# Kernel optimization log

Measured on AMD Instinct MI355X. Metric: run time of the kernel, lower is better.

Reference implementation:

```python
import jax, jax.numpy as jnp
import numpy as np

FEAT = 256
HID = 256
HEADS = 4
DH = HID // HEADS
SCALE = DH ** (-0.5)


def _linear(x, W, b):
    # torch nn.Linear convention: W is [out, in]
    return jnp.einsum('...i,oi->...o', x, W) + b


def _layernorm(x, gamma, beta, eps=1e-5):
    mu = jnp.mean(x, axis=-1, keepdims=True)
    var = jnp.mean(jnp.square(x - mu), axis=-1, keepdims=True)
    return (x - mu) * jax.lax.rsqrt(var + eps) * gamma + beta


def setup_inputs() -> dict:
    key = jax.random.key(0)
    ks = jax.random.split(key, 16)
    B, N = 4, 2048
    def w(k, shape, fan_in):
        return jax.random.uniform(k, shape, jnp.float32, -1.0, 1.0) / np.sqrt(fan_in)
    return {
        'x0': jax.random.normal(ks[0], (B, N, FEAT), jnp.float32),
        'x1': jax.random.normal(ks[1], (B, N, FEAT), jnp.float32),
        'Wqk': w(ks[2], (HID, FEAT), FEAT), 'bqk': w(ks[3], (HID,), FEAT),
        'Wv': w(ks[4], (HID, FEAT), FEAT), 'bv': w(ks[5], (HID,), FEAT),
        'Wp': w(ks[6], (HID, HID), HID), 'bp': w(ks[7], (HID,), HID),
        'W1': w(ks[8], (FEAT * 2, FEAT + HID), FEAT + HID), 'b1': w(ks[9], (FEAT * 2,), FEAT + HID),
        'gamma': jnp.ones((FEAT * 2,), jnp.float32), 'beta': jnp.zeros((FEAT * 2,), jnp.float32),
        'W2': w(ks[10], (FEAT, FEAT * 2), FEAT * 2), 'b2': w(ks[11], (FEAT,), FEAT * 2),
    }


def _forward(x0, x1, Wqk, bqk, Wv, bv, Wp, bp, W1, b1, gamma, beta, W2, b2):
    B, N0, _ = x0.shape
    N1 = x1.shape[1]

    def heads(t):  # [B, N, HID] -> [B, H, N, DH]
        return t.reshape(t.shape[0], t.shape[1], HEADS, DH).transpose(0, 2, 1, 3)

    qk0 = heads(_linear(x0, Wqk, bqk)) * (SCALE ** 0.5)
    qk1 = heads(_linear(x1, Wqk, bqk)) * (SCALE ** 0.5)
    v0 = heads(_linear(x0, Wv, bv))
    v1 = heads(_linear(x1, Wv, bv))

    sim = jnp.einsum('bhid,bhjd->bhij', qk0, qk1)  # [B,H,N0,N1]
    attn01 = jax.nn.softmax(sim, axis=-1)                      # rows over N1
    attn10 = jax.nn.softmax(sim.transpose(0, 1, 3, 2), axis=-1)  # [B,H,N1,N0], rows over N0

    m0 = jnp.einsum('bhij,bhjd->bhid', attn01, v1)  # [B,H,N0,DH]
    m1 = jnp.einsum('bhij,bhjd->bhid', attn10, v0)  # [B,H,N1,DH]

    def merge(t):  # [B,H,N,DH] -> [B,N,HID]
        return t.transpose(0, 2, 1, 3).reshape(t.shape[0], t.shape[2], HID)

    m0 = _linear(merge(m0), Wp, bp)
    m1 = _linear(merge(m1), Wp, bp)

    def mlp(x, m):
        h = _linear(jnp.concatenate([x, m], axis=-1), W1, b1)
        h = jax.nn.gelu(_layernorm(h, gamma, beta), approximate=False)
        return x + _linear(h, W2, b2)

    return mlp(x0, m0), mlp(x1, m1)


def reference(x0, x1, Wqk, bqk, Wv, bv, Wp, bp, W1, b1, gamma, beta, W2, b2):
    return _forward(x0, x1, Wqk, bqk, Wv, bv, Wp, bp, W1, b1, gamma, beta, W2, b2)
```

## Files before the change

### kernel.cpp

```cpp
#include <hip/hip_runtime.h>
#include <hip/hip_bf16.h>
#include <math.h>

typedef __hip_bfloat16 hbf;
typedef __attribute__((ext_vector_type(8))) short short8;
typedef __attribute__((ext_vector_type(4))) short short4v;
typedef __attribute__((ext_vector_type(4))) float f32x4;

#define ROWS 8192
#define SQSL 0.4246609001440095f
#define COFF 24.0f

__device__ __forceinline__ short f2b(float f) {
    union { hbf h; short s; } u; u.h = __float2bfloat16(f); return u.s;
}
__device__ __forceinline__ float b2f(short s) {
    union { unsigned u; float f; } x;
    x.u = ((unsigned)(unsigned short)s) << 16; return x.f;
}

__global__ __launch_bounds__(256)
void prep(const float* __restrict__ Wqk, const float* __restrict__ Wv,
          const float* __restrict__ Wp, const float* __restrict__ W1,
          const float* __restrict__ W2,
          const float* __restrict__ bp, const float* __restrict__ b1,
          short* __restrict__ wq, short* __restrict__ wv,
          short* __restrict__ w1c, short* __restrict__ w2,
          float* __restrict__ bc)
{
    const int bid = blockIdx.x, tid = threadIdx.x;
    if (bid < 512) {
        const float* src; short* dst; int base; float sc = 1.f;
        if (bid < 64)       { src = Wqk; dst = wq; base = bid;       sc = SQSL; }
        else if (bid < 128) { src = Wv;  dst = wv; base = bid - 64; }
        else if (bid < 384) {
            int i = (bid - 128) * 256 + tid;
            int n = i >> 7, c = (i & 127) * 4;
            if (c < 256) {
                float4 f = ((const float4*)W1)[i];
                short4v s;
                s[0] = f2b(f.x); s[1] = f2b(f.y); s[2] = f2b(f.z); s[3] = f2b(f.w);
                *(short4v*)(w1c + (size_t)n * 512 + c) = s;
            }
            return;
        }
        else                { src = W2;  dst = w2; base = bid - 384; }
        int i = base * 256 + tid;
        float4 f = ((const float4*)src)[i];
        short4v s;
        s[0] = f2b(f.x * sc); s[1] = f2b(f.y * sc);
        s[2] = f2b(f.z * sc); s[3] = f2b(f.w * sc);
        *(short4v*)(dst + (size_t)i * 4) = s;
    } else if (bid < 1024) {
        int n = bid - 512;
        const float* wrow = W1 + (size_t)n * 512 + 256;
        float acc = 0.f;
        for (int k = 0; k < 256; ++k)
            acc += wrow[k] * Wp[(size_t)k * 256 + tid];
        w1c[(size_t)n * 512 + 256 + tid] = f2b(acc);
    } else {
        int n = (bid - 1024) * 256 + tid;
        const float* wrow = W1 + (size_t)n * 512 + 256;
        float acc = b1[n];
        for (int k = 0; k < 256; ++k) acc += wrow[k] * bp[k];
        bc[n] = acc;
    }
}

__global__ __launch_bounds__(256)
void gemm_qkv(const float* __restrict__ x0, const float* __restrict__ x1,
              const short* __restrict__ Wa, const short* __restrict__ Wb,
              const float* __restrict__ bias0, const float* __restrict__ bias1,
              short* __restrict__ qkb, short* __restrict__ vtb)
{
    const int fid  = blockIdx.x + (blockIdx.y << 2);
    const int col0 = (fid >> 8) * 128;
    const int row0 = (fid & 255) * 64;
    const int tid = threadIdx.x;
    const int lane = tid & 63, wave = tid >> 6;
    const int ln = lane & 15, quad = lane >> 4;
    const int wm = wave & 1, wn = wave >> 1;

    __shared__ short smem[64 * 72 + 128 * 72];
    short* As = smem;
    short* Bs = smem + 64 * 72;
    short* Vt = smem;

    const int ar = tid >> 2, ac = tid & 3;

    f32x4 acc[2][4];
    #pragma unroll
    for (int i = 0; i < 2; ++i)
        #pragma unroll
        for (int j = 0; j < 4; ++j) acc[i][j] = {0.f, 0.f, 0.f, 0.f};

    const short* wbase = (col0 < 256) ? Wa + (size_t)col0 * 256
                                      : Wb + (size_t)(col0 - 256) * 256;
    const float* xrow = (row0 + ar < ROWS)
        ? x0 + (size_t)(row0 + ar) * 256
        : x1 + (size_t)(row0 + ar - ROWS) * 256;

    float4 aF[4];
    short8 bR[4];
    #pragma unroll
    for (int i = 0; i < 4; ++i) aF[i] = ((const float4*)(xrow + ac * 16))[i];
    bR[0] = *(const short8*)(wbase + (size_t)ar * 256 + ac * 16);
    bR[1] = *(const short8*)(wbase + (size_t)ar * 256 + ac * 16 + 8);
    bR[2] = *(const short8*)(wbase + (size_t)(ar + 64) * 256 + ac * 16);
    bR[3] = *(const short8*)(wbase + (size_t)(ar + 64) * 256 + ac * 16 + 8);

    for (int k0 = 0; k0 < 256; k0 += 64) {
        {
            short8 s0, s1;
            s0[0] = f2b(aF[0].x); s0[1] = f2b(aF[0].y); s0[2] = f2b(aF[0].z); s0[3] = f2b(aF[0].w);
            s0[4] = f2b(aF[1].x); s0[5] = f2b(aF[1].y); s0[6] = f2b(aF[1].z); s0[7] = f2b(aF[1].w);
            s1[0] = f2b(aF[2].x); s1[1] = f2b(aF[2].y); s1[2] = f2b(aF[2].z); s1[3] = f2b(aF[2].w);
            s1[4] = f2b(aF[3].x); s1[5] = f2b(aF[3].y); s1[6] = f2b(aF[3].z); s1[7] = f2b(aF[3].w);
            *(short8*)&As[ar * 72 + ac * 16]     = s0;
            *(short8*)&As[ar * 72 + ac * 16 + 8] = s1;
        }
        *(short8*)&Bs[ar * 72 + ac * 16]            = bR[0];
        *(short8*)&Bs[ar * 72 + ac * 16 + 8]        = bR[1];
        *(short8*)&Bs[(ar + 64) * 72 + ac * 16]     = bR[2];
        *(short8*)&Bs[(ar + 64) * 72 + ac * 16 + 8] = bR[3];
        __syncthreads();

        if (k0 + 64 < 256) {
            const int kk = k0 + 64 + ac * 16;
            #pragma unroll
            for (int i = 0; i < 4; ++i) aF[i] = ((const float4*)(xrow + kk))[i];
            bR[0] = *(const short8*)(wbase + (size_t)ar * 256 + kk);
            bR[1] = *(const short8*)(wbase + (size_t)ar * 256 + kk + 8);
            bR[2] = *(const short8*)(wbase + (size_t)(ar + 64) * 256 + kk);
            bR[3] = *(const short8*)(wbase + (size_t)(ar + 64) * 256 + kk + 8);
        }

        short8 a[2][2], b[4][2];
        #pragma unroll
        for (int mi = 0; mi < 2; ++mi)
            #pragma unroll
            for (int ks = 0; ks < 2; ++ks)
                a[mi][ks] = *(const short8*)&As[(wm * 32 + mi * 16 + ln) * 72 + ks * 32 + quad * 8];
        #pragma unroll
        for (int nj = 0; nj < 4; ++nj)
            #pragma unroll
            for (int ks = 0; ks < 2; ++ks)
                b[nj][ks] = *(const short8*)&Bs[(wn * 64 + nj * 16 + ln) * 72 + ks * 32 + quad * 8];
        #pragma unroll
        for (int mi = 0; mi < 2; ++mi)
            #pragma unroll
            for (int nj = 0; nj < 4; ++nj) {
                acc[mi][nj] = __builtin_amdgcn_mfma_f32_16x16x32_bf16(
                                  b[nj][0], a[mi][0], acc[mi][nj], 0, 0, 0);
                acc[mi][nj] = __builtin_amdgcn_mfma_f32_16x16x32_bf16(
                                  b[nj][1], a[mi][1], acc[mi][nj], 0, 0, 0);
            }
        __syncthreads();
    }

    if (col0 < 256) {
        #pragma unroll
        for (int nj = 0; nj < 4; ++nj) {
            const int wcol = col0 + wn * 64 + nj * 16 + quad * 4;
            float4 bb = *(const float4*)(bias0 + wcol);
            #pragma unroll
            for (int mi = 0; mi < 2; ++mi) {
                const int tok = row0 + wm * 32 + mi * 16 + ln;
                f32x4 v = acc[mi][nj];
                short4v o;
                o[0] = f2b(fmaf(bb.x, SQSL, v[0]));
                o[1] = f2b(fmaf(bb.y, SQSL, v[1]));
                o[2] = f2b(fmaf(bb.z, SQSL, v[2]));
                o[3] = f2b(fmaf(bb.w, SQSL, v[3]));
                *(short4v*)(qkb + (size_t)tok * 256 + wcol) = o;
            }
        }
    } else {
        #pragma unroll
        for (int nj = 0; nj < 4; ++nj) {
            const int wrel = wn * 64 + nj * 16 + quad * 4;
            float4 bb = *(const float4*)(bias1 + (col0 - 256) + wrel);
            #pragma unroll
            for (int mi = 0; mi < 2; ++mi) {
                const int tl = wm * 32 + mi * 16 + ln;
                f32x4 v = acc[mi][nj];
                Vt[(wrel + 0) * 72 + tl] = f2b(v[0] + bb.x);
                Vt[(wrel + 1) * 72 + tl] = f2b(v[1] + bb.y);
                Vt[(wrel + 2) * 72 + tl] = f2b(v[2] + bb.z);
                Vt[(wrel + 3) * 72 + tl] = f2b(v[3] + bb.w);
            }
        }
        __syncthreads();
        {
            const int g4 = (row0 >> 11) * 4, tc0 = row0 & 2047;
            const int r = tid >> 1, hf = tid & 1;
            const int vcol = (col0 - 256) + r;
            const int hh = vcol >> 6, d = vcol & 63;
            short* dst = vtb + (size_t)((g4 + hh) * 64 + d) * 2048 + tc0 + hf * 32;
            #pragma unroll
            for (int cc = 0; cc < 4; ++cc)
                *(short8*)(dst + cc * 8) = *(const short8*)&Vt[r * 72 + hf * 32 + cc * 8];
        }
    }
}

__global__ __launch_bounds__(128, 2)
void attn8(const short* __restrict__ qkb, const short* __restrict__ vtbuf,
           short* __restrict__ pO0, short* __restrict__ pO1,
           float* __restrict__ l0, float* __restrict__ l1)
{
    const int nfl = blockIdx.x + (blockIdx.y << 4) + (blockIdx.z << 8);
    const int qt  = nfl >> 6;
    const int gg  = nfl & 63;
    const int b    = (gg >> 2) & 3, h = gg & 3;
    const int dir  = gg >> 5;
    const int half = (gg >> 4) & 1;
    const int tid = threadIdx.x;
    const int lane = tid & 63, wave = tid >> 6;
    const int ln   = lane & 15, quad = lane >> 4;

    const int qbase = dir * ROWS + b * 2048;
    const int kbase = (1 - dir) * ROWS + b * 2048;
    const int vg    = ((1 - dir) * 4 + b) * 4 + h;
    const int jlo   = half * 1024, jhi = jlo + 1024;

    short* __restrict__ pO = half ? pO1 : pO0;
    float* __restrict__ lb = half ? l1  : l0;

    __shared__ short QP[128 * 72];
    __shared__ short KS[64 * 72];
    __shared__ short VT[64 * 72];

    const int c = tid & 7, r0 = tid >> 3;
    #pragma unroll
    for (int g = 0; g < 8; ++g) {
        int r = r0 + g * 16;
        *(short8*)&QP[r * 72 + c * 8] =
            *(const short8*)(qkb + (size_t)(qbase + qt * 128 + r) * 256 + h * 64 + c * 8);
    }
    #pragma unroll
    for (int g = 0; g < 4; ++g) {
        int r = r0 + g * 16;
        *(short8*)&KS[r * 72 + c * 8] =
            *(const short8*)(qkb + (size_t)(kbase + jlo + r) * 256 + h * 64 + c * 8);
        *(short8*)&VT[r * 72 + c * 8] =
            *(const short8*)(vtbuf + (size_t)(vg * 64 + r) * 2048 + jlo + c * 8);
    }
    __syncthreads();

    short8 qf[4][2];
    #pragma unroll
    for (int mi = 0; mi < 4; ++mi)
        #pragma unroll
        for (int ks = 0; ks < 2; ++ks)
            qf[mi][ks] = *(const short8*)&QP[(wave * 64 + mi * 16 + ln) * 72
                                             + ks * 32 + quad * 8];

    f32x4 Ot[4][4];
    #pragma unroll
    for (int mi = 0; mi < 4; ++mi)
        #pragma unroll
        for (int dt = 0; dt < 4; ++dt) Ot[mi][dt] = {0.f, 0.f, 0.f, 0.f};
    float lrun[4] = {0.f, 0.f, 0.f, 0.f};

    for (int j0 = jlo; j0 < jhi; j0 += 64) {
        short8 kreg[4], vreg[4];
        const bool more = (j0 + 64) < jhi;
        if (more) {
            #pragma unroll
            for (int g = 0; g < 4; ++g) {
                int r = r0 + g * 16;
                kreg[g] = *(const short8*)(qkb + (size_t)(kbase + j0 + 64 + r) * 256
                                           + h * 64 + c * 8);
                vreg[g] = *(const short8*)(vtbuf + (size_t)(vg * 64 + r) * 2048
                                           + j0 + 64 + c * 8);
            }
        }

        f32x4 St[4][4];
        __builtin_amdgcn_s_setprio(1);
        #pragma unroll
        for (int t = 0; t < 4; ++t) {
            short8 k0 = *(const short8*)&KS[(t * 16 + ln) * 72 + quad * 8];
            short8 k1 = *(const short8*)&KS[(t * 16 + ln) * 72 + 32 + quad * 8];
            #pragma unroll
            for (int mi = 0; mi < 4; ++mi) {
                f32x4 z = {0.f, 0.f, 0.f, 0.f};
                z = __builtin_amdgcn_mfma_f32_16x16x32_bf16(k0, qf[mi][0], z, 0, 0, 0);
                St[mi][t] = __builtin_amdgcn_mfma_f32_16x16x32_bf16(k1, qf[mi][1], z, 0, 0, 0);
            }
        }
        __builtin_amdgcn_s_setprio(0);

        float ss[4] = {0.f, 0.f, 0.f, 0.f};
        #pragma unroll
        for (int mi = 0; mi < 4; ++mi)
            #pragma unroll
            for (int t = 0; t < 4; ++t) {
                float p0 = __builtin_amdgcn_exp2f(St[mi][t][0] - COFF);
                float p1 = __builtin_amdgcn_exp2f(St[mi][t][1] - COFF);
                float p2 = __builtin_amdgcn_exp2f(St[mi][t][2] - COFF);
                float p3 = __builtin_amdgcn_exp2f(St[mi][t][3] - COFF);
                ss[mi] += (p0 + p1) + (p2 + p3);
                unsigned d0 = (__float_as_uint(p0) >> 16) |
                              (__float_as_uint(p1) & 0xffff0000u);
                unsigned d1 = (__float_as_uint(p2) >> 16) |
                              (__float_as_uint(p3) & 0xffff0000u);
                *(int2*)&QP[(wave * 64 + mi * 16 + ln) * 72 + t * 16 + quad * 4] =
                    make_int2((int)d0, (int)d1);
            }
        #pragma unroll
        for (int mi = 0; mi < 4; ++mi) {
            float t = ss[mi];
            t += __shfl_xor(t, 16);
            t += __shfl_xor(t, 32);
            lrun[mi] += t;
        }

        short8 pa[4][2];
        #pragma unroll
        for (int mi = 0; mi < 4; ++mi)
            #pragma unroll
            for (int ks = 0; ks < 2; ++ks)
                pa[mi][ks] = *(const short8*)&QP[(wave * 64 + mi * 16 + ln) * 72
                                                 + ks * 32 + quad * 8];
        __builtin_amdgcn_s_setprio(1);
        #pragma unroll
        for (int dt = 0; dt < 4; ++dt) {
            short8 v0 = *(const short8*)&VT[(dt * 16 + ln) * 72 + quad * 8];
            short8 v1 = *(const short8*)&VT[(dt * 16 + ln) * 72 + 32 + quad * 8];
            #pragma unroll
            for (int mi = 0; mi < 4; ++mi) {
                Ot[mi][dt] = __builtin_amdgcn_mfma_f32_16x16x32_bf16(
                                 v0, pa[mi][0], Ot[mi][dt], 0, 0, 0);
                Ot[mi][dt] = __builtin_amdgcn_mfma_f32_16x16x32_bf16(
                                 v1, pa[mi][1], Ot[mi][dt], 0, 0, 0);
            }
        }
        __builtin_amdgcn_s_setprio(0);
        __syncthreads();

        if (more) {
            #pragma unroll
            for (int g = 0; g < 4; ++g) {
                int r = r0 + g * 16;
                *(short8*)&KS[r * 72 + c * 8] = kreg[g];
                *(short8*)&VT[r * 72 + c * 8] = vreg[g];
            }
        }
        __syncthreads();
    }

    #pragma unroll
    for (int mi = 0; mi < 4; ++mi) {
        int tok = qbase + qt * 128 + wave * 64 + mi * 16 + ln;
        if (quad == 0) lb[tok] = lrun[mi];
        #pragma unroll
        for (int dt = 0; dt < 4; ++dt) {
            short4v o;
            #pragma unroll
            for (int r = 0; r < 4; ++r) o[r] = f2b(Ot[mi][dt][r]);
            *(short4v*)(pO + (size_t)tok * 256 + h * 64 + dt * 16 + quad * 4) = o;
        }
    }
}

__global__ __launch_bounds__(256)
void mlp_fused(const float* __restrict__ x0, const float* __restrict__ x1,
               const short* __restrict__ pO0, const short* __restrict__ pO1,
               const float* __restrict__ l0, const float* __restrict__ l1,
               const short* __restrict__ w1c, const short* __restrict__ w2,
               const float* __restrict__ bc, const float* __restrict__ gamma,
               const float* __restrict__ beta, const float* __restrict__ b2,
               float* __restrict__ out)
{
    const int tok0 = blockIdx.x * 32;
    const int tid = threadIdx.x;
    const int lane = tid & 63, wave = tid >> 6;
    const int ln = lane & 15, quad = lane >> 4;

    __shared__ short H [32 * 520];
    __shared__ short Bs[256 * 72];
    __shared__ float stats[4][2][32];

    const int br = tid >> 2, bq = tid & 3;
    short8 bp[8];
    auto loadB = [&](const short* W, int rw, int k0) {
        const short* src = W + (size_t)(rw + br) * 512 + k0 + bq * 16;
        #pragma unroll
        for (int q = 0; q < 4; ++q) {
            bp[2 * q]     = *(const short8*)(src + (size_t)q * 64 * 512);
            bp[2 * q + 1] = *(const short8*)(src + (size_t)q * 64 * 512 + 8);
        }
    };
    loadB(w1c, 0, 0);

    {
        const int arow = tid >> 3, ac = tid & 7;
        const int tok = tok0 + arow;
        if (ac < 4) {
            const float* xr = (tok < ROWS ? x0 + (size_t)tok * 256
                                          : x1 + (size_t)(tok - ROWS) * 256) + ac * 64;
            #pragma unroll
            for (int cc = 0; cc < 8; ++cc) {
                float4 f0 = ((const float4*)(xr + cc * 8))[0];
                float4 f1 = ((const float4*)(xr + cc * 8))[1];
                short8 s;
                s[0] = f2b(f0.x); s[1] = f2b(f0.y); s[2] = f2b(f0.z); s[3] = f2b(f0.w);
                s[4] = f2b(f1.x); s[5] = f2b(f1.y); s[6] = f2b(f1.z); s[7] = f2b(f1.w);
                *(short8*)&H[arow * 520 + ac * 64 + cc * 8] = s;
            }
        } else {
            const int vc = (ac - 4) * 64;
            const float inv = __builtin_amdgcn_rcpf(l0[tok] + l1[tok]);
            #pragma unroll
            for (int cc = 0; cc < 8; ++cc) {
                short8 a = *(const short8*)(pO0 + (size_t)tok * 256 + vc + cc * 8);
                short8 b = *(const short8*)(pO1 + (size_t)tok * 256 + vc + cc * 8);
                short8 s;
                #pragma unroll
                for (int j = 0; j < 8; ++j)
                    s[j] = f2b((b2f(a[j]) + b2f(b[j])) * inv);
                *(short8*)&H[arow * 520 + 256 + vc + cc * 8] = s;
            }
        }
    }

    f32x4 acc[2][8];
    #pragma unroll
    for (int i = 0; i < 2; ++i)
        #pragma unroll
        for (int j = 0; j < 8; ++j) acc[i][j] = {0.f, 0.f, 0.f, 0.f};

    __syncthreads();

    for (int k2 = 0; k2 < 8; ++k2) {
        const int k0 = k2 * 64;
        short8 a0[2], a1[2];
        #pragma unroll
        for (int ks = 0; ks < 2; ++ks) {
            a0[ks] = *(const short8*)&H[ln * 520 + k0 + ks * 32 + quad * 8];
            a1[ks] = *(const short8*)&H[(16 + ln) * 520 + k0 + ks * 32 + quad * 8];
        }
        #pragma unroll
        for (int p = 0; p < 2; ++p) {
            #pragma unroll
            for (int q = 0; q < 4; ++q) {
                *(short8*)&Bs[(br + q * 64) * 72 + bq * 16]     = bp[2 * q];
                *(short8*)&Bs[(br + q * 64) * 72 + bq * 16 + 8] = bp[2 * q + 1];
            }
            __syncthreads();
            if (p == 0)          loadB(w1c, 256, k0);
            else if (k2 < 7)     loadB(w1c, 0, k0 + 64);
            #pragma unroll
            for (int nj = 0; nj < 4; ++nj) {
                #pragma unroll
                for (int ks = 0; ks < 2; ++ks) {
                    short8 bf = *(const short8*)&Bs[(wave * 64 + nj * 16 + ln) * 72
                                                    + ks * 32 + quad * 8];
                    acc[0][p * 4 + nj] = __builtin_amdgcn_mfma_f32_16x16x32_bf16(
                                             bf, a0[ks], acc[0][p * 4 + nj], 0, 0, 0);
                    acc[1][p * 4 + nj] = __builtin_amdgcn_mfma_f32_16x16x32_bf16(
                                             bf, a1[ks], acc[1][p * 4 + nj], 0, 0, 0);
                }
            }
            __syncthreads();
        }
    }

    loadB(w2, 0, 0);

    #pragma unroll
    for (int p = 0; p < 2; ++p)
        #pragma unroll
        for (int nj = 0; nj < 4; ++nj) {
            int hcol = p * 256 + wave * 64 + nj * 16 + quad * 4;
            float4 bb = *(const float4*)(bc + hcol);
            acc[0][p * 4 + nj][0] += bb.x; acc[1][p * 4 + nj][0] += bb.x;
            acc[0][p * 4 + nj][1] += bb.y; acc[1][p * 4 + nj][1] += bb.y;
            acc[0][p * 4 + nj][2] += bb.z; acc[1][p * 4 + nj][2] += bb.z;
            acc[0][p * 4 + nj][3] += bb.w; acc[1][p * 4 + nj][3] += bb.w;
        }

    #pragma unroll
    for (int mi = 0; mi < 2; ++mi) {
        float s1 = 0.f, s2 = 0.f;
        #pragma unroll
        for (int j = 0; j < 8; ++j)
            #pragma unroll
            for (int r = 0; r < 4; ++r) {
                float v = acc[mi][j][r];
                s1 += v; s2 += v * v;
            }
        s1 += __shfl_xor(s1, 16); s2 += __shfl_xor(s2, 16);
        s1 += __shfl_xor(s1, 32); s2 += __shfl_xor(s2, 32);
        if (quad == 0) {
            stats[wave][0][mi * 16 + ln] = s1;
            stats[wave][1][mi * 16 + ln] = s2;
        }
    }
    __syncthreads();

    float mean[2], rstd[2];
    #pragma unroll
    for (int mi = 0; mi < 2; ++mi) {
        int t = mi * 16 + ln;
        float s1 = stats[0][0][t] + stats[1][0][t] + stats[2][0][t] + stats[3][0][t];
        float s2 = stats[0][1][t] + stats[1][1][t] + stats[2][1][t] + stats[3][1][t];
        mean[mi] = s1 * (1.f / 512.f);
        float var = s2 * (1.f / 512.f) - mean[mi] * mean[mi];
        rstd[mi] = rsqrtf(var + 1e-5f);
    }

    #pragma unroll
    for (int p = 0; p < 2; ++p)
        #pragma unroll
        for (int nj = 0; nj < 4; ++nj) {
            int hcol = p * 256 + wave * 64 + nj * 16 + quad * 4;
            float4 gm = *(const float4*)(gamma + hcol);
            float4 bt = *(const float4*)(beta + hcol);
            #pragma unroll
            for (int mi = 0; mi < 2; ++mi) {
                short4v o;
                #pragma unroll
                for (int r = 0; r < 4; ++r) {
                    float g = (r == 0) ? gm.x : (r == 1) ? gm.y : (r == 2) ? gm.z : gm.w;
                    float bta = (r == 0) ? bt.x : (r == 1) ? bt.y : (r == 2) ? bt.z : bt.w;
                    float y = (acc[mi][p * 4 + nj][r] - mean[mi]) * rstd[mi] * g + bta;
                    float u = y * fmaf(y * y, 0.0356774081f, 0.7978845608f);
                    float e = __builtin_amdgcn_exp2f(u * -2.8853900818f);
                    o[r] = f2b(y * __builtin_amdgcn_rcpf(1.f + e));
                }
                *(short4v*)&H[(mi * 16 + ln) * 520 + hcol] = o;
            }
        }

    f32x4 acc2[2][4];
    #pragma unroll
    for (int i = 0; i < 2; ++i)
        #pragma unroll
        for (int j = 0; j < 4; ++j) acc2[i][j] = {0.f, 0.f, 0.f, 0.f};

    for (int s = 0; s < 8; ++s) {
        const int k0 = s * 64;
        #pragma unroll
        for (int q = 0; q < 4; ++q) {
            *(short8*)&Bs[(br + q * 64) * 72 + bq * 16]     = bp[2 * q];
            *(short8*)&Bs[(br + q * 64) * 72 + bq * 16 + 8] = bp[2 * q + 1];
        }
        __syncthreads();
        if (s < 7) loadB(w2, 0, k0 + 64);
        short8 h0[2], h1[2];
        #pragma unroll
        for (int ks = 0; ks < 2; ++ks) {
            h0[ks] = *(const short8*)&H[ln * 520 + k0 + ks * 32 + quad * 8];
            h1[ks] = *(const short8*)&H[(16 + ln) * 520 + k0 + ks * 32 + quad * 8];
        }
        #pragma unroll
        for (int nj = 0; nj < 4; ++nj) {
            #pragma unroll
            for (int ks = 0; ks < 2; ++ks) {
                short8 wf = *(const short8*)&Bs[(wave * 64 + nj * 16 + ln) * 72
                                                + ks * 32 + quad * 8];
                acc2[0][nj] = __builtin_amdgcn_mfma_f32_16x16x32_bf16(
                                  wf, h0[ks], acc2[0][nj], 0, 0, 0);
                acc2[1][nj] = __builtin_amdgcn_mfma_f32_16x16x32_bf16(
                                  wf, h1[ks], acc2[1][nj], 0, 0, 0);
            }
        }
        __syncthreads();
    }

    #pragma unroll
    for (int nj = 0; nj < 4; ++nj) {
        int ocol = wave * 64 + nj * 16 + quad * 4;
        float4 bb = *(const float4*)(b2 + ocol);
        #pragma unroll
        for (int mi = 0; mi < 2; ++mi) {
            int tok = tok0 + mi * 16 + ln;
            const float* xr = (tok < ROWS ? x0 + (size_t)tok * 256
                                          : x1 + (size_t)(tok - ROWS) * 256);
            float4 rv = *(const float4*)(xr + ocol);
            float4 o;
            o.x = acc2[mi][nj][0] + bb.x + rv.x;
            o.y = acc2[mi][nj][1] + bb.y + rv.y;
            o.z = acc2[mi][nj][2] + bb.z + rv.z;
            o.w = acc2[mi][nj][3] + bb.w + rv.w;
            *(float4*)(out + (size_t)tok * 256 + ocol) = o;
        }
    }
}

extern "C" void kernel_launch(void* const* d_in, const int* in_sizes, int n_in,
                              void* d_out, int out_size, void* d_ws, size_t ws_size,
                              hipStream_t stream)
{
    const float* x0    = (const float*)d_in[0];
    const float* x1    = (const float*)d_in[1];
    const float* Wqk   = (const float*)d_in[2];
    const float* bqk   = (const float*)d_in[3];
    const float* Wv    = (const float*)d_in[4];
    const float* bv    = (const float*)d_in[5];
    const float* Wp    = (const float*)d_in[6];
    const float* bp    = (const float*)d_in[7];
    const float* W1    = (const float*)d_in[8];
    const float* b1    = (const float*)d_in[9];
    const float* gamma = (const float*)d_in[10];
    const float* beta  = (const float*)d_in[11];
    const float* W2    = (const float*)d_in[12];
    const float* b2    = (const float*)d_in[13];
    float* out = (float*)d_out;

    char* ws = (char*)d_ws;
    const size_t MB = 1024 * 1024;
    short* qkb  = (short*)ws;
    short* vtb  = (short*)(ws + 8  * MB);
    short* pO0  = (short*)(ws + 16 * MB);
    short* pO1  = (short*)(ws + 24 * MB);
    float* l0   = (float*)(ws + 32 * MB);
    float* l1   = l0 + 16384;
    float* bc   = l1 + 16384;
    short* wq   = (short*)(bc + 512);
    short* wv   = wq + 65536;
    short* w1c  = wv + 65536;
    short* w2   = w1c + 262144;

    prep<<<1026, 256, 0, stream>>>(Wqk, Wv, Wp, W1, W2, bp, b1,
                                   wq, wv, w1c, w2, bc);
    gemm_qkv<<<dim3(4, 256), 256, 0, stream>>>(x0, x1, wq, wv, bqk, bv, qkb, vtb);
    attn8<<<dim3(16, 16, 4), 128, 0, stream>>>(qkb, vtb, pO0, pO1, l0, l1);
    mlp_fused<<<512, 256, 0, stream>>>(x0, x1, pO0, pO1, l0, l1, w1c, w2, bc,
                                       gamma, beta, b2, out);
}
```

Before: 202.2 us.

## Compute softmax row sums via MFMA with ones vector and drop exp offset

Moves the per-row softmax denominator off the VALU: the bf16 probability fragments are multiplied against a vector of ones with extra MFMAs, replacing the scalar adds and cross-lane shuffles. The constant exponent offset (COFF) is removed, bf16 packing uses a byte-permute instruction, and the setprio hints around the MFMA blocks are dropped. Without the offset, large scores could overflow exp2 in fp32, and the row sums are now taken from the bf16-rounded probabilities rather than the fp32 values.

```diff
diff --git a/kernel.cpp b/kernel.cpp
--- a/kernel.cpp
+++ b/kernel.cpp
@@ -9,7 +9,6 @@
 
 #define ROWS 8192
 #define SQSL 0.4246609001440095f
-#define COFF 24.0f
 
 __device__ __forceinline__ short f2b(float f) {
     union { hbf h; short s; } u; u.h = __float2bfloat16(f); return u.s;
@@ -256,12 +255,18 @@
             qf[mi][ks] = *(const short8*)&QP[(wave * 64 + mi * 16 + ln) * 72
                                              + ks * 32 + quad * 8];
 
+    short8 ones;
+    #pragma unroll
+    for (int j = 0; j < 8; ++j) ones[j] = (short)0x3F80;
+
     f32x4 Ot[4][4];
     #pragma unroll
     for (int mi = 0; mi < 4; ++mi)
         #pragma unroll
         for (int dt = 0; dt < 4; ++dt) Ot[mi][dt] = {0.f, 0.f, 0.f, 0.f};
-    float lrun[4] = {0.f, 0.f, 0.f, 0.f};
+    f32x4 lacc[4];
+    #pragma unroll
+    for (int mi = 0; mi < 4; ++mi) lacc[mi] = {0.f, 0.f, 0.f, 0.f};
 
     for (int j0 = jlo; j0 < jhi; j0 += 64) {
         short8 kreg[4], vreg[4];
@@ -278,7 +283,6 @@
         }
 
         f32x4 St[4][4];
-        __builtin_amdgcn_s_setprio(1);
         #pragma unroll
         for (int t = 0; t < 4; ++t) {
             short8 k0 = *(const short8*)&KS[(t * 16 + ln) * 72 + quad * 8];
@@ -290,32 +294,22 @@
                 St[mi][t] = __builtin_amdgcn_mfma_f32_16x16x32_bf16(k1, qf[mi][1], z, 0, 0, 0);
             }
         }
-        __builtin_amdgcn_s_setprio(0);
-
-        float ss[4] = {0.f, 0.f, 0.f, 0.f};
+
         #pragma unroll
         for (int mi = 0; mi < 4; ++mi)
             #pragma unroll
             for (int t = 0; t < 4; ++t) {
-                float p0 = __builtin_amdgcn_exp2f(St[mi][t][0] - COFF);
-                float p1 = __builtin_amdgcn_exp2f(St[mi][t][1] - COFF);
-                float p2 = __builtin_amdgcn_exp2f(St[mi][t][2] - COFF);
-                float p3 = __builtin_amdgcn_exp2f(St[mi][t][3] - COFF);
-                ss[mi] += (p0 + p1) + (p2 + p3);
-                unsigned d0 = (__float_as_uint(p0) >> 16) |
-                              (__float_as_uint(p1) & 0xffff0000u);
-                unsigned d1 = (__float_as_uint(p2) >> 16) |
-                              (__float_as_uint(p3) & 0xffff0000u);
+                float p0 = __builtin_amdgcn_exp2f(St[mi][t][0]);
+                float p1 = __builtin_amdgcn_exp2f(St[mi][t][1]);
+                float p2 = __builtin_amdgcn_exp2f(St[mi][t][2]);
+                float p3 = __builtin_amdgcn_exp2f(St[mi][t][3]);
+                unsigned d0 = __builtin_amdgcn_perm(__float_as_uint(p1),
+                                                    __float_as_uint(p0), 0x07060302u);
+                unsigned d1 = __builtin_amdgcn_perm(__float_as_uint(p3),
+                                                    __float_as_uint(p2), 0x07060302u);
                 *(int2*)&QP[(wave * 64 + mi * 16 + ln) * 72 + t * 16 + quad * 4] =
                     make_int2((int)d0, (int)d1);
             }
-        #pragma unroll
-        for (int mi = 0; mi < 4; ++mi) {
-            float t = ss[mi];
-            t += __shfl_xor(t, 16);
-            t += __shfl_xor(t, 32);
-            lrun[mi] += t;
-        }
 
         short8 pa[4][2];
         #pragma unroll
@@ -324,7 +318,13 @@
             for (int ks = 0; ks < 2; ++ks)
                 pa[mi][ks] = *(const short8*)&QP[(wave * 64 + mi * 16 + ln) * 72
                                                  + ks * 32 + quad * 8];
-        __builtin_amdgcn_s_setprio(1);
+        #pragma unroll
+        for (int mi = 0; mi < 4; ++mi) {
+            lacc[mi] = __builtin_amdgcn_mfma_f32_16x16x32_bf16(
+                           ones, pa[mi][0], lacc[mi], 0, 0, 0);
+            lacc[mi] = __builtin_amdgcn_mfma_f32_16x16x32_bf16(
+                           ones, pa[mi][1], lacc[mi], 0, 0, 0);
+        }
         #pragma unroll
         for (int dt = 0; dt < 4; ++dt) {
             short8 v0 = *(const short8*)&VT[(dt * 16 + ln) * 72 + quad * 8];
@@ -337,7 +337,6 @@
                                  v1, pa[mi][1], Ot[mi][dt], 0, 0, 0);
             }
         }
-        __builtin_amdgcn_s_setprio(0);
         __syncthreads();
 
         if (more) {
@@ -354,7 +353,7 @@
     #pragma unroll
     for (int mi = 0; mi < 4; ++mi) {
         int tok = qbase + qt * 128 + wave * 64 + mi * 16 + ln;
-        if (quad == 0) lb[tok] = lrun[mi];
+        if (quad == 0) lb[tok] = lacc[mi][0];
         #pragma unroll
         for (int dt = 0; dt < 4; ++dt) {
             short4v o;
```

Measured after the change: 196.5 us. -2.8%, faster.
